# Kernel tuning notes

Hardware: AMD Instinct MI355X
Metric: run time of the kernel (lower is better)

Reference implementation:

```python
import jax, jax.numpy as jnp
import numpy as np

B, N, D = 128, 512, 128      # graphs, nodes/graph, feature dim
KEEP_RATIO = 0.5
K = int(KEEP_RATIO * N)      # kept nodes per graph (fixed -> jit friendly)
EDGE_P = 0.05                # random graph edge density


def setup_inputs() -> dict:
    key = jax.random.key(0)
    k1, k2, k3 = jax.random.split(key, 3)
    # random symmetric binary adjacency without self loops, per graph block
    u = jax.random.uniform(k1, (B, N, N))
    a0 = (u < EDGE_P).astype(jnp.float32)
    a0 = jnp.maximum(a0, jnp.swapaxes(a0, 1, 2))
    eye = jnp.eye(N, dtype=jnp.float32)
    a0 = a0 * (1.0 - eye)
    # normalized input adjacency: D^-0.5 (A0 + I) D^-0.5 (as `normalization` does)
    a_hat = a0 + eye
    dinv = a_hat.sum(-1) ** -0.5
    adjacency = a_hat * dinv[:, :, None] * dinv[:, None, :]   # [B,N,N]
    input_feature = jax.random.normal(k2, (B, N, D), dtype=jnp.float32)
    graph_indicator = jnp.repeat(jnp.arange(B, dtype=jnp.int32), N)  # [B*N]
    # attn_gcn params: Linear(D -> 1) kaiming-style init, zero bias
    weight = jax.random.normal(k3, (D, 1), dtype=jnp.float32) * (2.0 / D) ** 0.5
    bias = jnp.zeros((1,), dtype=jnp.float32)
    return {"adjacency": adjacency, "input_feature": input_feature,
            "graph_indicator": graph_indicator, "weight": weight, "bias": bias}


def reference(adjacency, input_feature, graph_indicator, weight, bias):
    # --- attention GCN: Z = A @ (X W) + b, then tanh ---
    support = jnp.einsum('bnd,do->bno', input_feature, weight)      # [B,N,1]
    score = jnp.einsum('bnm,bmo->bno', adjacency, support) + bias   # [B,N,1]
    attn = jnp.tanh(score[..., 0])                                  # [B,N]
    # --- top_rank: per-graph top-K by score; mask preserves node order ---
    _, idx = jax.lax.top_k(attn, K)                                 # [B,K]
    idx = jnp.sort(idx, axis=-1)                                    # original node order
    # --- hidden = X[mask] * attn[mask] ---
    kept_x = jnp.take_along_axis(input_feature, idx[:, :, None], axis=1)  # [B,K,D]
    kept_s = jnp.take_along_axis(attn, idx, axis=1)                       # [B,K]
    hidden = (kept_x * kept_s[:, :, None]).reshape(B * K, D)
    mask_graph_indicator = jnp.repeat(jnp.arange(B, dtype=graph_indicator.dtype), K)
    # --- filter_adjacency: binarize off-diagonal structure, gather, renormalize ---
    eye_n = jnp.eye(N, dtype=adjacency.dtype)
    a_bin = jnp.where((adjacency != 0) & (eye_n == 0), 1.0, 0.0)    # [B,N,N]
    rows = jnp.take_along_axis(a_bin, idx[:, :, None], axis=1)      # [B,K,N]
    sub = jnp.take_along_axis(rows, idx[:, None, :], axis=2)        # [B,K,K]
    a_hat = sub + jnp.eye(K, dtype=adjacency.dtype)
    dinv = a_hat.sum(-1) ** -0.5
    mask_adjacency = a_hat * dinv[:, :, None] * dinv[:, None, :]    # [B,K,K]
    return hidden, mask_graph_indicator, mask_adjacency
```

## Files before the change

### kernel.cpp

```cpp
#include <hip/hip_runtime.h>
#include <hip/hip_bf16.h>
#include <math.h>

#define BGR 128
#define NND 512
#define DFD 128
#define KKP 256

__global__ __launch_bounds__(256) void k_support(const float* __restrict__ X,
                                                 const float* __restrict__ W,
                                                 float* __restrict__ sup) {
    __shared__ float w_s[DFD];
    int t = threadIdx.x;
    if (t < DFD) w_s[t] = W[t];
    __syncthreads();
    int node = blockIdx.x * 64 + (t >> 2);
    int q = t & 3;
    const float4* xp = (const float4*)(X + (size_t)node * DFD + q * 32);
    const float4* wp = (const float4*)(w_s + q * 32);
    float sum = 0.f;
#pragma unroll
    for (int i = 0; i < 8; ++i) {
        float4 x = xp[i], w = wp[i];
        sum += x.x * w.x + x.y * w.y + x.z * w.z + x.w * w.w;
    }
    sum += __shfl_xor(sum, 1);
    sum += __shfl_xor(sum, 2);
    if (q == 0) sup[node] = sum;
}

__global__ __launch_bounds__(256) void k_score(const float* __restrict__ A,
                                               const float* __restrict__ sup,
                                               const float* __restrict__ bias,
                                               float* __restrict__ attn) {
    __shared__ float sup_s[NND];
    int b = blockIdx.x >> 6;
    int rblk = blockIdx.x & 63;
    int t = threadIdx.x;
    sup_s[t] = sup[b * NND + t];
    sup_s[256 + t] = sup[b * NND + 256 + t];
    __syncthreads();
    int wave = t >> 6, l = t & 63;
    float bias0 = bias[0];
    const float4* sp = (const float4*)sup_s;
    float4 s0 = sp[l], s1 = sp[64 + l];
#pragma unroll
    for (int r = 0; r < 2; ++r) {
        int row = rblk * 8 + wave * 2 + r;
        const float4* ap = (const float4*)(A + ((size_t)b * NND + row) * NND);
        float4 a0 = ap[l], a1 = ap[64 + l];
        float sum = a0.x * s0.x + a0.y * s0.y + a0.z * s0.z + a0.w * s0.w
                  + a1.x * s1.x + a1.y * s1.y + a1.z * s1.z + a1.w * s1.w;
#pragma unroll
        for (int off = 32; off >= 1; off >>= 1) sum += __shfl_down(sum, off);
        if (l == 0) attn[b * NND + row] = tanhf(sum + bias0);
    }
}

__global__ __launch_bounds__(256) void k_topk(const float* __restrict__ X,
                                              const float* __restrict__ attn,
                                              float* __restrict__ out_hidden,
                                              float* __restrict__ out_gi,
                                              int* __restrict__ gidx) {
    __shared__ float attn_s[NND];
    __shared__ unsigned int km[16];
    __shared__ int idx_s[KKP];
    int b = blockIdx.x, t = threadIdx.x;
    attn_s[t] = attn[b * NND + t];
    attn_s[256 + t] = attn[b * NND + 256 + t];
    __syncthreads();
    int wave = t >> 6, l = t & 63;

    float a0 = attn_s[t], a1 = attn_s[t + 256];
    int r0 = 0, r1 = 0;
    for (int j = 0; j < NND; ++j) {
        float v = attn_s[j];
        r0 += (v > a0 || (v == a0 && j < t)) ? 1 : 0;
        r1 += (v > a1 || (v == a1 && j < t + 256)) ? 1 : 0;
    }
    bool keep0 = r0 < KKP, keep1 = r1 < KKP;

    unsigned long long m0 = __ballot(keep0);
    unsigned long long m1 = __ballot(keep1);
    if (l == 0) {
        km[wave * 2]     = (unsigned int)m0;
        km[wave * 2 + 1] = (unsigned int)(m0 >> 32);
        km[8 + wave * 2]     = (unsigned int)m1;
        km[8 + wave * 2 + 1] = (unsigned int)(m1 >> 32);
    }
    __syncthreads();

#pragma unroll
    for (int h = 0; h < 2; ++h) {
        int i = t + 256 * h;
        bool kp = h == 0 ? keep0 : keep1;
        if (kp) {
            int w = i >> 5;
            int pos = 0;
            for (int u = 0; u < w; ++u) pos += __popc(km[u]);
            pos += __popc(km[w] & ((1u << (i & 31)) - 1u));
            idx_s[pos] = i;
            gidx[b * KKP + pos] = i;
        }
    }
    out_gi[b * KKP + t] = (float)b;
    __syncthreads();

    for (int r = 0; r < 64; ++r) {
        int k = wave * 64 + r;
        int node = idx_s[k];
        float s = attn_s[node];
        const float2* xp = (const float2*)(X + ((size_t)b * NND + node) * DFD);
        float2 v = xp[l];
        v.x *= s; v.y *= s;
        ((float2*)(out_hidden + ((size_t)b * KKP + k) * DFD))[l] = v;
    }
}

__global__ __launch_bounds__(256) void k_bits(const float* __restrict__ A,
                                              const int* __restrict__ gidx,
                                              unsigned int* __restrict__ bits,
                                              float* __restrict__ dinv) {
    __shared__ int idx_s[KKP];
    __shared__ float rowbuf[4][NND];
    int b = blockIdx.x >> 3, blk = blockIdx.x & 7;
    int t = threadIdx.x, wave = t >> 6, l = t & 63;
    idx_s[t] = gidx[b * KKP + t];
    __syncthreads();
    for (int r = 0; r < 8; ++r) {
        int i = blk * 32 + wave * 8 + r;
        int node = idx_s[i];
        const float4* ap = (const float4*)(A + ((size_t)b * NND + node) * NND);
        float4 v0 = ap[l], v1 = ap[64 + l];
        ((float4*)(rowbuf[wave]))[l] = v0;
        ((float4*)(rowbuf[wave]))[64 + l] = v1;
        __syncthreads();
        int rowsum = 1;
        unsigned long long masks[4];
#pragma unroll
        for (int c = 0; c < 4; ++c) {
            int j = c * 64 + l;
            bool bit = (j != i) && (rowbuf[wave][idx_s[j]] != 0.0f);
            masks[c] = __ballot(bit);
            rowsum += __popcll(masks[c]);
        }
        if (l == 0) {
            size_t base = ((size_t)b * KKP + i) * 8;
#pragma unroll
            for (int c = 0; c < 4; ++c) {
                bits[base + 2 * c]     = (unsigned int)masks[c];
                bits[base + 2 * c + 1] = (unsigned int)(masks[c] >> 32);
            }
            dinv[b * KKP + i] = 1.0f / sqrtf((float)rowsum);
        }
        __syncthreads();
    }
}

__global__ __launch_bounds__(256) void k_norm(const unsigned int* __restrict__ bits,
                                              const float* __restrict__ dinv,
                                              float* __restrict__ out_adj) {
    __shared__ float dinv_s[KKP];
    int b = blockIdx.x >> 5;
    int rblk = blockIdx.x & 31;
    int t = threadIdx.x, wave = t >> 6, l = t & 63;
    dinv_s[t] = dinv[b * KKP + t];
    __syncthreads();
    float4 dj = ((const float4*)dinv_s)[l];
    const float* djp = &dj.x;
#pragma unroll
    for (int r = 0; r < 2; ++r) {
        int i = rblk * 8 + wave * 2 + r;
        float di = dinv_s[i];
        const unsigned int* bp = bits + ((size_t)b * KKP + i) * 8;
        unsigned int word = bp[l >> 3];
        int j0 = l * 4;
        float4 v;
        float* pv = &v.x;
#pragma unroll
        for (int c = 0; c < 4; ++c) {
            int j = j0 + c;
            float ah = ((word >> (j & 31)) & 1u) ? 1.0f : 0.0f;
            if (j == i) ah += 1.0f;
            pv[c] = ah * di * djp[c];
        }
        ((float4*)(out_adj + ((size_t)b * KKP + i) * KKP))[l] = v;
    }
}

extern "C" void kernel_launch(void* const* d_in, const int* in_sizes, int n_in,
                              void* d_out, int out_size, void* d_ws, size_t ws_size,
                              hipStream_t stream) {
    const float* A    = (const float*)d_in[0];
    const float* X    = (const float*)d_in[1];
    const float* W    = (const float*)d_in[3];
    const float* bias = (const float*)d_in[4];

    float* out        = (float*)d_out;
    float* out_hidden = out;
    float* out_gi     = out + (size_t)BGR * KKP * DFD;
    float* out_adj    = out_gi + (size_t)BGR * KKP;

    float* sup  = (float*)d_ws;
    float* attn = sup + (size_t)BGR * NND;
    int*   gidx = (int*)(attn + (size_t)BGR * NND);
    float* dinv = (float*)(gidx + (size_t)BGR * KKP);
    unsigned int* bits = (unsigned int*)(dinv + (size_t)BGR * KKP);

    k_support<<<BGR * NND / 64, 256, 0, stream>>>(X, W, sup);
    k_score<<<BGR * 64, 256, 0, stream>>>(A, sup, bias, attn);
    k_topk<<<BGR, 256, 0, stream>>>(X, attn, out_hidden, out_gi, gidx);
    k_bits<<<BGR * 8, 256, 0, stream>>>(A, gidx, bits, dinv);
    k_norm<<<BGR * 32, 256, 0, stream>>>(bits, dinv, out_adj);
}
```

Before: 81.49 us.

## Build adjacency bitmask during score pass and fuse topk with bit extraction

The score kernel now ballots the nonzero off-diagonal pattern of each adjacency row into a 512-bit mask while it already streams A, so A no longer has to be re-read to build the kept submatrix. The topk, gather and bit-extraction kernels are merged into one 512-thread-per-graph kernel that ranks nodes, gathers kept mask rows into LDS, extracts the KxK bits, computes dinv and writes the hidden features. This removes a second pass over a large fraction of A and one launch, but concentrates the work in only 128 blocks and adds extra ballot work and mask writes to the score kernel.

```diff
diff --git a/kernel.cpp b/kernel.cpp
--- a/kernel.cpp
+++ b/kernel.cpp
@@ -6,6 +6,9 @@
 #define NND 512
 #define DFD 128
 #define KKP 256
+
+typedef unsigned int uint;
+typedef unsigned long long ull;
 
 __global__ __launch_bounds__(256) void k_support(const float* __restrict__ X,
                                                  const float* __restrict__ W,
@@ -32,7 +35,8 @@
 __global__ __launch_bounds__(256) void k_score(const float* __restrict__ A,
                                                const float* __restrict__ sup,
                                                const float* __restrict__ bias,
-                                               float* __restrict__ attn) {
+                                               float* __restrict__ attn,
+                                               ull* __restrict__ bm) {
     __shared__ float sup_s[NND];
     int b = blockIdx.x >> 6;
     int rblk = blockIdx.x & 63;
@@ -51,63 +55,105 @@
         float4 a0 = ap[l], a1 = ap[64 + l];
         float sum = a0.x * s0.x + a0.y * s0.y + a0.z * s0.z + a0.w * s0.w
                   + a1.x * s1.x + a1.y * s1.y + a1.z * s1.z + a1.w * s1.w;
+        int c0 = 4 * l;
+        ull m[8];
+        m[0] = __ballot(a0.x != 0.f && (c0 + 0) != row);
+        m[1] = __ballot(a0.y != 0.f && (c0 + 1) != row);
+        m[2] = __ballot(a0.z != 0.f && (c0 + 2) != row);
+        m[3] = __ballot(a0.w != 0.f && (c0 + 3) != row);
+        m[4] = __ballot(a1.x != 0.f && (256 + c0 + 0) != row);
+        m[5] = __ballot(a1.y != 0.f && (256 + c0 + 1) != row);
+        m[6] = __ballot(a1.z != 0.f && (256 + c0 + 2) != row);
+        m[7] = __ballot(a1.w != 0.f && (256 + c0 + 3) != row);
 #pragma unroll
         for (int off = 32; off >= 1; off >>= 1) sum += __shfl_down(sum, off);
-        if (l == 0) attn[b * NND + row] = tanhf(sum + bias0);
-    }
-}
-
-__global__ __launch_bounds__(256) void k_topk(const float* __restrict__ X,
+        if (l == 0) {
+            attn[b * NND + row] = tanhf(sum + bias0);
+            ull* bp = bm + ((size_t)b * NND + row) * 8;
+#pragma unroll
+            for (int k = 0; k < 8; ++k) bp[k] = m[k];
+        }
+    }
+}
+
+__global__ __launch_bounds__(512) void k_fuse(const float* __restrict__ X,
                                               const float* __restrict__ attn,
+                                              const uint* __restrict__ bm,
                                               float* __restrict__ out_hidden,
                                               float* __restrict__ out_gi,
-                                              int* __restrict__ gidx) {
+                                              uint* __restrict__ bits,
+                                              float* __restrict__ dinv) {
     __shared__ float attn_s[NND];
-    __shared__ unsigned int km[16];
+    __shared__ uint km[16];
     __shared__ int idx_s[KKP];
+    __shared__ uint4 bm_s4[KKP][4];
+    __shared__ uint bits_s[KKP][8];
     int b = blockIdx.x, t = threadIdx.x;
     attn_s[t] = attn[b * NND + t];
-    attn_s[256 + t] = attn[b * NND + 256 + t];
     __syncthreads();
     int wave = t >> 6, l = t & 63;
 
-    float a0 = attn_s[t], a1 = attn_s[t + 256];
-    int r0 = 0, r1 = 0;
-    for (int j = 0; j < NND; ++j) {
-        float v = attn_s[j];
-        r0 += (v > a0 || (v == a0 && j < t)) ? 1 : 0;
-        r1 += (v > a1 || (v == a1 && j < t + 256)) ? 1 : 0;
-    }
-    bool keep0 = r0 < KKP, keep1 = r1 < KKP;
-
-    unsigned long long m0 = __ballot(keep0);
-    unsigned long long m1 = __ballot(keep1);
-    if (l == 0) {
-        km[wave * 2]     = (unsigned int)m0;
-        km[wave * 2 + 1] = (unsigned int)(m0 >> 32);
-        km[8 + wave * 2]     = (unsigned int)m1;
-        km[8 + wave * 2 + 1] = (unsigned int)(m1 >> 32);
-    }
-    __syncthreads();
-
-#pragma unroll
-    for (int h = 0; h < 2; ++h) {
-        int i = t + 256 * h;
-        bool kp = h == 0 ? keep0 : keep1;
-        if (kp) {
-            int w = i >> 5;
-            int pos = 0;
-            for (int u = 0; u < w; ++u) pos += __popc(km[u]);
-            pos += __popc(km[w] & ((1u << (i & 31)) - 1u));
-            idx_s[pos] = i;
-            gidx[b * KKP + pos] = i;
+    float a = attn_s[t];
+    int r = 0;
+    const float4* ap4 = (const float4*)attn_s;
+    for (int jj = 0; jj < 128; ++jj) {
+        float4 v = ap4[jj];
+        int j0 = jj * 4;
+        r += (v.x > a || (v.x == a && j0     < t)) ? 1 : 0;
+        r += (v.y > a || (v.y == a && j0 + 1 < t)) ? 1 : 0;
+        r += (v.z > a || (v.z == a && j0 + 2 < t)) ? 1 : 0;
+        r += (v.w > a || (v.w == a && j0 + 3 < t)) ? 1 : 0;
+    }
+    bool keep = r < KKP;
+    ull mk = __ballot(keep);
+    if (l == 0) { km[wave * 2] = (uint)mk; km[wave * 2 + 1] = (uint)(mk >> 32); }
+    __syncthreads();
+    if (keep) {
+        int w = t >> 5, pos = 0;
+        for (int u = 0; u < w; ++u) pos += __popc(km[u]);
+        pos += __popc(km[w] & ((1u << (t & 31)) - 1u));
+        idx_s[pos] = t;
+    }
+    if (t < KKP) out_gi[b * KKP + t] = (float)b;
+    __syncthreads();
+
+    {
+        int i = t >> 1, half = t & 1;
+        const uint4* src = (const uint4*)(bm + ((size_t)b * NND + idx_s[i]) * 16) + half * 2;
+        bm_s4[i][half * 2]     = src[0];
+        bm_s4[i][half * 2 + 1] = src[1];
+    }
+    __syncthreads();
+
+    const uint* bmw = (const uint*)bm_s4;
+    int j = t & 255;
+    int jn = idx_s[j];
+    int widx = ((jn >> 8) * 4 + (jn & 3)) * 2 + ((jn >> 7) & 1);
+    int bitpos = (jn >> 2) & 31;
+    int rowoff = t >> 8;
+    int wq = (t >> 6) & 3;
+    for (int ii = 0; ii < KKP; ii += 2) {
+        int row = ii + rowoff;
+        uint kb = (bmw[row * 16 + widx] >> bitpos) & 1u;
+        ull mb = __ballot(kb != 0u);
+        if (l == 0) {
+            bits_s[row][wq * 2]     = (uint)mb;
+            bits_s[row][wq * 2 + 1] = (uint)(mb >> 32);
+            uint* gp = bits + ((size_t)b * KKP + row) * 8 + wq * 2;
+            gp[0] = (uint)mb;
+            gp[1] = (uint)(mb >> 32);
         }
     }
-    out_gi[b * KKP + t] = (float)b;
-    __syncthreads();
-
-    for (int r = 0; r < 64; ++r) {
-        int k = wave * 64 + r;
+    __syncthreads();
+    if (t < KKP) {
+        int s = 1;
+#pragma unroll
+        for (int k = 0; k < 8; ++k) s += __popc(bits_s[t][k]);
+        dinv[b * KKP + t] = 1.0f / sqrtf((float)s);
+    }
+
+    for (int r2 = 0; r2 < 32; ++r2) {
+        int k = wave * 32 + r2;
         int node = idx_s[k];
         float s = attn_s[node];
         const float2* xp = (const float2*)(X + ((size_t)b * NND + node) * DFD);
@@ -117,47 +163,7 @@
     }
 }
 
-__global__ __launch_bounds__(256) void k_bits(const float* __restrict__ A,
-                                              const int* __restrict__ gidx,
-                                              unsigned int* __restrict__ bits,
-                                              float* __restrict__ dinv) {
-    __shared__ int idx_s[KKP];
-    __shared__ float rowbuf[4][NND];
-    int b = blockIdx.x >> 3, blk = blockIdx.x & 7;
-    int t = threadIdx.x, wave = t >> 6, l = t & 63;
-    idx_s[t] = gidx[b * KKP + t];
-    __syncthreads();
-    for (int r = 0; r < 8; ++r) {
-        int i = blk * 32 + wave * 8 + r;
-        int node = idx_s[i];
-        const float4* ap = (const float4*)(A + ((size_t)b * NND + node) * NND);
-        float4 v0 = ap[l], v1 = ap[64 + l];
-        ((float4*)(rowbuf[wave]))[l] = v0;
-        ((float4*)(rowbuf[wave]))[64 + l] = v1;
-        __syncthreads();
-        int rowsum = 1;
-        unsigned long long masks[4];
-#pragma unroll
-        for (int c = 0; c < 4; ++c) {
-            int j = c * 64 + l;
-            bool bit = (j != i) && (rowbuf[wave][idx_s[j]] != 0.0f);
-            masks[c] = __ballot(bit);
-            rowsum += __popcll(masks[c]);
-        }
-        if (l == 0) {
-            size_t base = ((size_t)b * KKP + i) * 8;
-#pragma unroll
-            for (int c = 0; c < 4; ++c) {
-                bits[base + 2 * c]     = (unsigned int)masks[c];
-                bits[base + 2 * c + 1] = (unsigned int)(masks[c] >> 32);
-            }
-            dinv[b * KKP + i] = 1.0f / sqrtf((float)rowsum);
-        }
-        __syncthreads();
-    }
-}
-
-__global__ __launch_bounds__(256) void k_norm(const unsigned int* __restrict__ bits,
+__global__ __launch_bounds__(256) void k_norm(const uint* __restrict__ bits,
                                               const float* __restrict__ dinv,
                                               float* __restrict__ out_adj) {
     __shared__ float dinv_s[KKP];
@@ -172,8 +178,8 @@
     for (int r = 0; r < 2; ++r) {
         int i = rblk * 8 + wave * 2 + r;
         float di = dinv_s[i];
-        const unsigned int* bp = bits + ((size_t)b * KKP + i) * 8;
-        unsigned int word = bp[l >> 3];
+        const uint* bp = bits + ((size_t)b * KKP + i) * 8;
+        uint word = bp[l >> 3];
         int j0 = l * 4;
         float4 v;
         float* pv = &v.x;
@@ -203,13 +209,12 @@
 
     float* sup  = (float*)d_ws;
     float* attn = sup + (size_t)BGR * NND;
-    int*   gidx = (int*)(attn + (size_t)BGR * NND);
-    float* dinv = (float*)(gidx + (size_t)BGR * KKP);
-    unsigned int* bits = (unsigned int*)(dinv + (size_t)BGR * KKP);
+    ull*   bm   = (ull*)(attn + (size_t)BGR * NND);
+    uint*  bits = (uint*)(bm + (size_t)BGR * NND * 8);
+    float* dinv = (float*)(bits + (size_t)BGR * KKP * 8);
 
     k_support<<<BGR * NND / 64, 256, 0, stream>>>(X, W, sup);
-    k_score<<<BGR * 64, 256, 0, stream>>>(A, sup, bias, attn);
-    k_topk<<<BGR, 256, 0, stream>>>(X, attn, out_hidden, out_gi, gidx);
-    k_bits<<<BGR * 8, 256, 0, stream>>>(A, gidx, bits, dinv);
+    k_score<<<BGR * 64, 256, 0, stream>>>(A, sup, bias, attn, bm);
+    k_fuse<<<BGR, 512, 0, stream>>>(X, attn, (const uint*)bm, out_hidden, out_gi, bits, dinv);
     k_norm<<<BGR * 32, 256, 0, stream>>>(bits, dinv, out_adj);
 }
```

Result: faster. 71.01 us (-12.9%).
